# Kernel optimization log

Measured on AMD Instinct MI355X. Metric: run time of the kernel, lower is better.

Reference implementation:

```python
import jax, jax.numpy as jnp
import numpy as np

H = 8
DH = 64  # attention_head_size
HID = 512
NEG = -90000000000.0

def _lin(x, w, b):
    return x @ w + b

def _tfs(x):  # [N, HID] -> [H, N, DH]
    n = x.shape[0]
    return x.reshape(n, H, DH).transpose(1, 0, 2)

def _cross(q, ck, v, cv, mask, dw, db):
    # q: [H,N,DH], ck/cv: [H,M,DH], v: [H,N,DH], mask: [N,M]
    s = jnp.einsum('hnd,hmd->hnm', q, ck)
    s = s * mask[None, :, :] / jnp.sqrt(jnp.asarray(DH, s.dtype))
    s = jnp.where(s == 0.0, NEG, s)  # faithful zero->-inf hack
    p = jax.nn.softmax(s, axis=-1)
    ctx = v + jnp.einsum('hnm,hmd->hnd', p, cv)  # residual add of raw value
    n = ctx.shape[1]
    ctx = ctx.transpose(1, 0, 2).reshape(n, H * DH)
    return _lin(ctx, dw, db)

def setup_inputs() -> dict:
    key = jax.random.key(0)
    ks = jax.random.split(key, 24)
    N1, N2, D1 = 4096, 4096, 300
    d = {}
    d['h_head'] = jax.random.normal(ks[0], (N1, D1), jnp.float32)
    d['h_tail'] = jax.random.normal(ks[1], (N2, HID), jnp.float32)
    d['batch_head'] = jnp.sort(jax.random.randint(ks[2], (N1,), 0, 64))
    d['batch_tail'] = jnp.sort(jax.random.randint(ks[3], (N2,), 0, 64))
    def w(k, i, o):
        return jax.random.normal(k, (i, o), jnp.float32) / np.sqrt(i)
    d['map_w'] = w(ks[4], D1, HID); d['map_b'] = jnp.zeros((HID,), jnp.float32)
    names = ['q1', 'k1', 'v1', 'q2', 'k2', 'v2', 'd1', 'd2']
    for i, nm in enumerate(names):
        d[nm + '_w'] = w(ks[5 + i], HID, HID)
        d[nm + '_b'] = jnp.zeros((HID,), jnp.float32)
    return d

def reference(h_head, h_tail, batch_head, batch_tail,
              map_w, map_b,
              q1_w, q1_b, k1_w, k1_b, v1_w, v1_b,
              q2_w, q2_b, k2_w, k2_b, v2_w, v2_b,
              d1_w, d1_b, d2_w, d2_b):
    hh = _lin(h_head, map_w, map_b)  # n_dim1 != n_dim2 -> map
    q_h = _tfs(_lin(hh, q1_w, q1_b))
    k_h = _tfs(_lin(hh, k1_w, k1_b))
    v_h = _tfs(_lin(hh, v1_w, v1_b))
    q_t = _tfs(_lin(h_tail, q2_w, q2_b))
    k_t = _tfs(_lin(h_tail, k2_w, k2_b))
    v_t = _tfs(_lin(h_tail, v2_w, v2_b))
    mask = (batch_head[:, None] == batch_tail[None, :]).astype(jnp.float32)
    out_head = _cross(q_h, k_t, v_h, v_t, mask, d1_w, d1_b)
    out_tail = _cross(q_t, k_h, v_t, v_h, mask.T, d2_w, d2_b)
    return (out_head, out_tail)
```

## Files before the change

### kernel.cpp

```cpp
#include <hip/hip_runtime.h>
#include <hip/hip_bf16.h>
#include <math.h>


typedef __bf16 bf16x8 __attribute__((ext_vector_type(8)));
typedef float  f32x4  __attribute__((ext_vector_type(4)));

#define HID 512
#define NTOK 4096

#define AS1(p) ((const __attribute__((address_space(1))) void*)(p))
#define AS3(p) ((__attribute__((address_space(3))) void*)(p))

__device__ __forceinline__ void fold_tile(
    const float* __restrict__ Wf,
    const float* __restrict__ Mw,
    __bf16* __restrict__ F,
    int bx, int by, char* SMEM)
{
    __bf16* As = (__bf16*)SMEM;
    __bf16* Bs = (__bf16*)(SMEM + 8192);

    const int tid  = threadIdx.x;
    const int wave = tid >> 6;
    const int lane = tid & 63;
    const int quad = lane >> 4;
    const int l16  = lane & 15;
    const int wy   = wave >> 1;
    const int wx   = wave & 1;
    const int rowBase = by * 128;
    const int colBase = bx * 128;

    const int s_row = tid >> 2;
    const int s_gc  = (tid & 3) ^ ((s_row >> 1) & 3);
    const int a_jj  = tid >> 3;
    const int a_c16 = (tid & 7) * 16;
    const int a_cp  = a_jj >> 3;
    const int a_sub = a_jj & 7;

    f32x4 acc[4][4] = {};

    for (int i = 0; i < 16; ++i) {
        const int j0 = i * 32;
        __syncthreads();
        #pragma unroll
        for (int h = 0; h < 2; ++h) {
            int r = s_row + h * 64;
            int k = colBase + r;
            bf16x8 v;
            if (k < 300) {
                const float* p = &Mw[(size_t)k * 512 + j0 + s_gc * 8];
                float4 f0 = *(const float4*)p;
                float4 f1 = *(const float4*)(p + 4);
                v[0]=(__bf16)f0.x; v[1]=(__bf16)f0.y; v[2]=(__bf16)f0.z; v[3]=(__bf16)f0.w;
                v[4]=(__bf16)f1.x; v[5]=(__bf16)f1.y; v[6]=(__bf16)f1.z; v[7]=(__bf16)f1.w;
            } else {
                #pragma unroll
                for (int u = 0; u < 8; ++u) v[u] = (__bf16)0.f;
            }
            *(bf16x8*)&Bs[h * 2048 + tid * 8] = v;
        }
        {
            const float* p = &Wf[(size_t)(j0 + a_jj) * 512 + rowBase + a_c16];
            float4 f0 = *(const float4*)p;
            float4 f1 = *(const float4*)(p + 4);
            float4 f2 = *(const float4*)(p + 8);
            float4 f3 = *(const float4*)(p + 12);
            float vals[16] = {f0.x,f0.y,f0.z,f0.w, f1.x,f1.y,f1.z,f1.w,
                              f2.x,f2.y,f2.z,f2.w, f3.x,f3.y,f3.z,f3.w};
            #pragma unroll
            for (int u = 0; u < 16; ++u) {
                int r  = a_c16 + u;
                int cp = a_cp ^ ((r >> 1) & 3);
                As[r * 32 + cp * 8 + a_sub] = (__bf16)vals[u];
            }
        }
        __syncthreads();

        bf16x8 ar[4], br[4];
        #pragma unroll
        for (int ii = 0; ii < 4; ++ii) {
            const int ra = wy * 64 + ii * 16 + l16;
            ar[ii] = *(const bf16x8*)&As[ra * 32 + ((quad ^ ((ra >> 1) & 3)) << 3)];
        }
        #pragma unroll
        for (int jj = 0; jj < 4; ++jj) {
            const int rb = wx * 64 + jj * 16 + l16;
            br[jj] = *(const bf16x8*)&Bs[rb * 32 + ((quad ^ ((rb >> 1) & 3)) << 3)];
        }
        #pragma unroll
        for (int ii = 0; ii < 4; ++ii)
            #pragma unroll
            for (int jj = 0; jj < 4; ++jj)
                acc[ii][jj] = __builtin_amdgcn_mfma_f32_16x16x32_bf16(ar[ii], br[jj], acc[ii][jj], 0, 0, 0);
    }

    #pragma unroll
    for (int jj = 0; jj < 4; ++jj) {
        int col = colBase + wx * 64 + jj * 16 + l16;
        if (col < 320) {
            #pragma unroll
            for (int ii = 0; ii < 4; ++ii) {
                #pragma unroll
                for (int r = 0; r < 4; ++r) {
                    int row = rowBase + wy * 64 + ii * 16 + quad * 4 + r;
                    F[(size_t)row * 320 + col] = (__bf16)acc[ii][jj][r];
                }
            }
        }
    }
}

struct PrepArgs {
    const float* h_head; const float* h_tail;
    const int* bh; const int* bt;
    const float* map_w; const float* map_b;
    const float* qkvw[3]; const float* qkvb[3];
    const float* tsrc[5]; __bf16* tdst[5];
    __bf16* hh_bf; __bf16* ht_bf;
    __bf16* F[3];
    float* fb;
    int* ranges;
};

__global__ __launch_bounds__(256) void fused_prep(PrepArgs pa) {
    const int q = blockIdx.x, z = blockIdx.z, tid = threadIdx.x;
    __shared__ __align__(16) char SMEM[32768];

    if (z == 0) {
        if (q == 0 && tid < 128) {
            int b = tid & 63;
            const int* arr = (tid < 64) ? pa.bh : pa.bt;
            int base = (tid < 64) ? 0 : 128;
            int lo = 0, hi = NTOK;
            while (lo < hi) { int mid = (lo + hi) >> 1; if (arr[mid] < b) lo = mid + 1; else hi = mid; }
            int start = lo;
            lo = 0; hi = NTOK;
            while (lo < hi) { int mid = (lo + hi) >> 1; if (arr[mid] <= b) lo = mid + 1; else hi = mid; }
            pa.ranges[base + b] = start;
            pa.ranges[base + 64 + b] = lo;
        }
        for (int idx = tid; idx < 8 * 40; idx += 256) {
            int r   = q * 8 + idx / 40;
            int col = (idx % 40) * 8;
            bf16x8 v;
            if (col + 8 <= 300) {
                float4 f0 = *(const float4*)&pa.h_head[(size_t)r * 300 + col];
                float4 f1 = *(const float4*)&pa.h_head[(size_t)r * 300 + col + 4];
                v[0]=(__bf16)f0.x; v[1]=(__bf16)f0.y; v[2]=(__bf16)f0.z; v[3]=(__bf16)f0.w;
                v[4]=(__bf16)f1.x; v[5]=(__bf16)f1.y; v[6]=(__bf16)f1.z; v[7]=(__bf16)f1.w;
            } else if (col < 300) {
                float4 f0 = *(const float4*)&pa.h_head[(size_t)r * 300 + col];
                v[0]=(__bf16)f0.x; v[1]=(__bf16)f0.y; v[2]=(__bf16)f0.z; v[3]=(__bf16)f0.w;
                v[4]=(__bf16)0.f; v[5]=(__bf16)0.f; v[6]=(__bf16)0.f; v[7]=(__bf16)0.f;
            } else {
                #pragma unroll
                for (int j = 0; j < 8; ++j) v[j] = (__bf16)0.f;
            }
            *(bf16x8*)&pa.hh_bf[(size_t)r * 320 + col] = v;
        }
    } else if (z == 1) {
        for (int idx = tid; idx < 8 * 64; idx += 256) {
            int r   = q * 8 + (idx >> 6);
            int col = (idx & 63) * 8;
            float4 f0 = *(const float4*)&pa.h_tail[(size_t)r * 512 + col];
            float4 f1 = *(const float4*)&pa.h_tail[(size_t)r * 512 + col + 4];
            bf16x8 v;
            v[0]=(__bf16)f0.x; v[1]=(__bf16)f0.y; v[2]=(__bf16)f0.z; v[3]=(__bf16)f0.w;
            v[4]=(__bf16)f1.x; v[5]=(__bf16)f1.y; v[6]=(__bf16)f1.z; v[7]=(__bf16)f1.w;
            *(bf16x8*)&pa.ht_bf[(size_t)r * 512 + col] = v;
        }
    } else if (z == 2) {
        if (q >= 24) return;
        float* red = (float*)SMEM;
        const int w  = q >> 3;
        const int c8 = q & 7;
        const int n  = c8 * 64 + (tid & 63);
        const int jq = tid >> 6;
        const float* W = pa.qkvw[w];
        float s = 0.f;
        for (int j = jq * 128; j < jq * 128 + 128; ++j)
            s += pa.map_b[j] * W[(size_t)j * 512 + n];
        red[tid] = s;
        __syncthreads();
        if (tid < 64) {
            float r4 = red[tid] + red[64 + tid] + red[128 + tid] + red[192 + tid]
                     + pa.qkvb[w][c8 * 64 + tid];
            pa.fb[w * 512 + c8 * 64 + tid] = r4;
        }
    } else if (z == 3) {
        if (q >= 36) return;
        const int f = q / 12, t = q % 12;
        fold_tile(pa.qkvw[f], pa.map_w, pa.F[f], t % 3, t / 3, SMEM);
    } else {
        if (q >= 64) return;
        typedef __bf16 trow[72];
        trow* T = (trow*)SMEM;
        const int jz = z - 4;
        const float* src = pa.tsrc[jz];
        __bf16* dst = pa.tdst[jz];
        const int tk = (q >> 3) * 64;
        const int tn = (q & 7) * 64;
        const int r0 = tid >> 4;
        const int c0 = (tid & 15) * 4;
        #pragma unroll
        for (int i = 0; i < 4; ++i) {
            float4 v = *(const float4*)&src[(size_t)(tk + r0 + i * 16) * 512 + tn + c0];
            T[r0 + i * 16][c0 + 0] = (__bf16)v.x;
            T[r0 + i * 16][c0 + 1] = (__bf16)v.y;
            T[r0 + i * 16][c0 + 2] = (__bf16)v.z;
            T[r0 + i * 16][c0 + 3] = (__bf16)v.w;
        }
        __syncthreads();
        const int n  = tid >> 2;
        const int kk = (tid & 3) * 16;
        bf16x8 o0, o1;
        #pragma unroll
        for (int j = 0; j < 8; ++j) { o0[j] = T[kk + j][n]; o1[j] = T[kk + 8 + j][n]; }
        __bf16* dp = dst + (size_t)(tn + n) * 512 + tk + kk;
        *(bf16x8*)dp       = o0;
        *(bf16x8*)(dp + 8) = o1;
    }
}

struct GemmJobs {
    const __bf16* A[6];
    const __bf16* W[6];
    const float*  bias[6];
    void*         C[6];
    int           Kp[6];
};

template <typename TC>
__global__ __launch_bounds__(256) void gemm128(GemmJobs jobs) {
    __shared__ __align__(16) __bf16 As[2][4096];
    __shared__ __align__(16) __bf16 Bs[2][4096];

    const int z = blockIdx.z;
    const __bf16* A    = jobs.A[z];
    const __bf16* W    = jobs.W[z];
    const float*  bias = jobs.bias[z];
    TC*           C    = (TC*)jobs.C[z];
    const int     Kp   = jobs.Kp[z];

    const int tid  = threadIdx.x;
    const int wave = tid >> 6;
    const int lane = tid & 63;
    const int quad = lane >> 4;
    const int l16  = lane & 15;
    const int wy   = wave >> 1;
    const int wx   = wave & 1;
    const int rowBase = blockIdx.y * 128;
    const int colBase = blockIdx.x * 128;

    const int s_row = tid >> 2;
    const int s_kc  = ((tid & 3) ^ ((s_row >> 1) & 3)) * 8;

    const __bf16* gA = A + (size_t)(rowBase + s_row) * Kp + s_kc;
    const __bf16* gB = W + (size_t)(colBase + s_row) * Kp + s_kc;
    const int waveOff = wave * 512;

    f32x4 acc[4][4] = {};
    const int nk = Kp >> 5;

    __builtin_amdgcn_global_load_lds(AS1(gA),                   AS3(&As[0][waveOff]),        16, 0, 0);
    __builtin_amdgcn_global_load_lds(AS1(gA + (size_t)64 * Kp), AS3(&As[0][2048 + waveOff]), 16, 0, 0);
    __builtin_amdgcn_global_load_lds(AS1(gB),                   AS3(&Bs[0][waveOff]),        16, 0, 0);
    __builtin_amdgcn_global_load_lds(AS1(gB + (size_t)64 * Kp), AS3(&Bs[0][2048 + waveOff]), 16, 0, 0);

    for (int i = 0; i < nk; ++i) {
        const int cur = i & 1;
        __syncthreads();

        if (i + 1 < nk) {
            const int kt = (i + 1) * 32;
            const int nx = cur ^ 1;
            __builtin_amdgcn_global_load_lds(AS1(gA + kt),                   AS3(&As[nx][waveOff]),        16, 0, 0);
            __builtin_amdgcn_global_load_lds(AS1(gA + kt + (size_t)64 * Kp), AS3(&As[nx][2048 + waveOff]), 16, 0, 0);
            __builtin_amdgcn_global_load_lds(AS1(gB + kt),                   AS3(&Bs[nx][waveOff]),        16, 0, 0);
            __builtin_amdgcn_global_load_lds(AS1(gB + kt + (size_t)64 * Kp), AS3(&Bs[nx][2048 + waveOff]), 16, 0, 0);
        }

        bf16x8 ar[4], br[4];
        #pragma unroll
        for (int ii = 0; ii < 4; ++ii) {
            const int ra = wy * 64 + ii * 16 + l16;
            ar[ii] = *(const bf16x8*)&As[cur][ra * 32 + ((quad ^ ((ra >> 1) & 3)) << 3)];
        }
        #pragma unroll
        for (int jj = 0; jj < 4; ++jj) {
            const int rb = wx * 64 + jj * 16 + l16;
            br[jj] = *(const bf16x8*)&Bs[cur][rb * 32 + ((quad ^ ((rb >> 1) & 3)) << 3)];
        }
        #pragma unroll
        for (int ii = 0; ii < 4; ++ii)
            #pragma unroll
            for (int jj = 0; jj < 4; ++jj)
                acc[ii][jj] = __builtin_amdgcn_mfma_f32_16x16x32_bf16(ar[ii], br[jj], acc[ii][jj], 0, 0, 0);
    }

    #pragma unroll
    for (int jj = 0; jj < 4; ++jj) {
        int col = colBase + wx * 64 + jj * 16 + l16;
        float bv = bias[col];
        #pragma unroll
        for (int ii = 0; ii < 4; ++ii) {
            #pragma unroll
            for (int r = 0; r < 4; ++r) {
                int row = rowBase + wy * 64 + ii * 16 + quad * 4 + r;
                C[(size_t)row * HID + col] = (TC)(acc[ii][jj][r] + bv);
            }
        }
    }
}

__global__ __launch_bounds__(256) void attn_mfma(
    const __bf16* __restrict__ Q0, const __bf16* __restrict__ K0,
    const __bf16* __restrict__ Vr0, const __bf16* __restrict__ Vc0,
    const __bf16* __restrict__ Q1, const __bf16* __restrict__ K1,
    const __bf16* __restrict__ Vr1, const __bf16* __restrict__ Vc1,
    const int* __restrict__ ranges,
    __bf16* __restrict__ O0, __bf16* __restrict__ O1,
    int Nq, int Nk)
{
    __shared__ __align__(16) __bf16 Qs[64][72];
    __shared__ __align__(16) __bf16 Ks[64][72];
    __shared__ __align__(16) __bf16 Vt[64][72];
    __shared__ __align__(16) __bf16 Ps[64][72];

    const int z = blockIdx.z;
    const __bf16* Q    = z ? Q1 : Q0;
    const __bf16* Kg   = z ? K1 : K0;
    const __bf16* Vres = z ? Vr1 : Vr0;
    const __bf16* Vctx = z ? Vc1 : Vc0;
    __bf16* Out        = z ? O1 : O0;
    const int* qstart  = z ? ranges + 128 : ranges;
    const int* qend    = z ? ranges + 192 : ranges + 64;
    const int* kstart  = z ? ranges       : ranges + 128;
    const int* kend    = z ? ranges + 64  : ranges + 192;

    const int h = blockIdx.x, b = blockIdx.y;
    const int qs = qstart[b], qe = qend[b];
    const int ts = kstart[b], te = kend[b];
    const int nq = qe - qs, nk = te - ts;
    if (nq <= 0) return;

    const int tid  = threadIdx.x;
    const int wave = tid >> 6;
    const int lane = tid & 63;
    const int quad = lane >> 4;
    const int l16  = lane & 15;
    const int srow = tid >> 2;
    const int scol = (tid & 3) * 16;

    if (nk <= 0) {
        float* meanv = (float*)Qs;
        if (tid < 64) {
            float s = 0.f;
            for (int m = 0; m < Nk; ++m)
                s += (float)Vctx[(size_t)m * HID + h * 64 + tid];
            meanv[tid] = s / (float)Nk;
        }
        __syncthreads();
        int d = tid & 63;
        for (int r = qs + (tid >> 6); r < qe; r += 4) {
            size_t off = (size_t)r * HID + h * 64 + d;
            Out[off] = (__bf16)((float)Vres[off] + meanv[d]);
        }
        return;
    }

    for (int qc = 0; qc < nq; qc += 64) {
        __syncthreads();
        {
            int qg = min(qs + qc + srow, Nq - 1);
            const __bf16* src = Q + (size_t)qg * HID + h * 64 + scol;
            *(bf16x8*)&Qs[srow][scol]     = *(const bf16x8*)src;
            *(bf16x8*)&Qs[srow][scol + 8] = *(const bf16x8*)(src + 8);
        }
        __syncthreads();
        bf16x8 aq0 = *(const bf16x8*)&Qs[wave * 16 + l16][quad * 8];
        bf16x8 aq1 = *(const bf16x8*)&Qs[wave * 16 + l16][32 + quad * 8];

        f32x4 O[4] = {};
        float Mx[4], L[4];
        #pragma unroll
        for (int r = 0; r < 4; ++r) { Mx[r] = -__builtin_inff(); L[r] = 0.f; }

        for (int kc = 0; kc < nk; kc += 64) {
            __syncthreads();
            {
                int kg = min(ts + kc + srow, Nk - 1);
                const __bf16* ksrc = Kg + (size_t)kg * HID + h * 64 + scol;
                *(bf16x8*)&Ks[srow][scol]     = *(const bf16x8*)ksrc;
                *(bf16x8*)&Ks[srow][scol + 8] = *(const bf16x8*)(ksrc + 8);
                const __bf16* vsrc = Vctx + (size_t)kg * HID + h * 64 + scol;
                bf16x8 v0 = *(const bf16x8*)vsrc;
                bf16x8 v1 = *(const bf16x8*)(vsrc + 8);
                #pragma unroll
                for (int j = 0; j < 8; ++j) {
                    Vt[scol + j][srow]     = v0[j];
                    Vt[scol + 8 + j][srow] = v1[j];
                }
            }
            __syncthreads();

            f32x4 S[4] = {};
            #pragma unroll
            for (int c = 0; c < 4; ++c) {
                bf16x8 bk0 = *(const bf16x8*)&Ks[c * 16 + l16][quad * 8];
                bf16x8 bk1 = *(const bf16x8*)&Ks[c * 16 + l16][32 + quad * 8];
                S[c] = __builtin_amdgcn_mfma_f32_16x16x32_bf16(aq0, bk0, S[c], 0, 0, 0);
                S[c] = __builtin_amdgcn_mfma_f32_16x16x32_bf16(aq1, bk1, S[c], 0, 0, 0);
            }

            #pragma unroll
            for (int c = 0; c < 4; ++c) {
                bool valid = (ts + kc + c * 16 + l16) < te;
                #pragma unroll
                for (int r = 0; r < 4; ++r)
                    S[c][r] = valid ? S[c][r] * 0.125f : -__builtin_inff();
            }

            float cm[4], ps[4], alpha[4];
            #pragma unroll
            for (int r = 0; r < 4; ++r) {
                float v = fmaxf(fmaxf(S[0][r], S[1][r]), fmaxf(S[2][r], S[3][r]));
                v = fmaxf(v, __shfl_xor(v, 1, 64));
                v = fmaxf(v, __shfl_xor(v, 2, 64));
                v = fmaxf(v, __shfl_xor(v, 4, 64));
                v = fmaxf(v, __shfl_xor(v, 8, 64));
                cm[r] = v;
            }
            #pragma unroll
            for (int r = 0; r < 4; ++r) {
                float nM = fmaxf(Mx[r], cm[r]);
                alpha[r] = __expf(Mx[r] - nM);
                Mx[r] = nM;
                ps[r] = 0.f;
            }
            #pragma unroll
            for (int c = 0; c < 4; ++c)
                #pragma unroll
                for (int r = 0; r < 4; ++r) {
                    float p = __expf(S[c][r] - Mx[r]);
                    S[c][r] = p;
                    ps[r] += p;
                }
            #pragma unroll
            for (int r = 0; r < 4; ++r) {
                float v = ps[r];
                v += __shfl_xor(v, 1, 64);
                v += __shfl_xor(v, 2, 64);
                v += __shfl_xor(v, 4, 64);
                v += __shfl_xor(v, 8, 64);
                L[r] = L[r] * alpha[r] + v;
            }
            #pragma unroll
            for (int c = 0; c < 4; ++c)
                #pragma unroll
                for (int r = 0; r < 4; ++r)
                    O[c][r] *= alpha[r];

            #pragma unroll
            for (int c = 0; c < 4; ++c)
                #pragma unroll
                for (int r = 0; r < 4; ++r)
                    Ps[wave * 16 + quad * 4 + r][c * 16 + l16] = (__bf16)S[c][r];
            __syncthreads();

            bf16x8 ap0 = *(const bf16x8*)&Ps[wave * 16 + l16][quad * 8];
            bf16x8 ap1 = *(const bf16x8*)&Ps[wave * 16 + l16][32 + quad * 8];
            #pragma unroll
            for (int c = 0; c < 4; ++c) {
                bf16x8 bv0 = *(const bf16x8*)&Vt[c * 16 + l16][quad * 8];
                bf16x8 bv1 = *(const bf16x8*)&Vt[c * 16 + l16][32 + quad * 8];
                O[c] = __builtin_amdgcn_mfma_f32_16x16x32_bf16(ap0, bv0, O[c], 0, 0, 0);
                O[c] = __builtin_amdgcn_mfma_f32_16x16x32_bf16(ap1, bv1, O[c], 0, 0, 0);
            }
        }

        #pragma unroll
        for (int c = 0; c < 4; ++c) {
            int d = h * 64 + c * 16 + l16;
            #pragma unroll
            for (int r = 0; r < 4; ++r) {
                int qrow = qs + qc + wave * 16 + quad * 4 + r;
                if (qrow < qe) {
                    size_t off = (size_t)qrow * HID + d;
                    Out[off] = (__bf16)((float)Vres[off] + O[c][r] / L[r]);
                }
            }
        }
    }
}

extern "C" void kernel_launch(void* const* d_in, const int* in_sizes, int n_in,
                              void* d_out, int out_size, void* d_ws, size_t ws_size,
                              hipStream_t stream) {
    (void)in_sizes; (void)n_in; (void)out_size; (void)ws_size;

    const float* h_head = (const float*)d_in[0];
    const float* h_tail = (const float*)d_in[1];
    const int* batch_head = (const int*)d_in[2];
    const int* batch_tail = (const int*)d_in[3];
    const float* map_w = (const float*)d_in[4];
    const float* map_b = (const float*)d_in[5];
    const float* q1_w = (const float*)d_in[6];
    const float* q1_b = (const float*)d_in[7];
    const float* k1_w = (const float*)d_in[8];
    const float* k1_b = (const float*)d_in[9];
    const float* v1_w = (const float*)d_in[10];
    const float* v1_b = (const float*)d_in[11];
    const float* q2_w = (const float*)d_in[12];
    const float* q2_b = (const float*)d_in[13];
    const float* k2_w = (const float*)d_in[14];
    const float* k2_b = (const float*)d_in[15];
    const float* v2_w = (const float*)d_in[16];
    const float* v2_b = (const float*)d_in[17];
    const float* d1_w = (const float*)d_in[18];
    const float* d1_b = (const float*)d_in[19];
    const float* d2_w = (const float*)d_in[20];
    const float* d2_b = (const float*)d_in[21];

    float* out = (float*)d_out;

    const size_t SZ = (size_t)NTOK * HID;
    char* ws = (char*)d_ws;
    int* ranges   = (int*)ws;
    __bf16* hh_bf = (__bf16*)(ws + 1024);
    __bf16* ht_bf = hh_bf + (size_t)NTOK * 320;
    __bf16* q2T  = ht_bf + SZ;
    __bf16* k2T  = q2T + 512 * 512;
    __bf16* v2T  = k2T + 512 * 512;
    __bf16* d1T  = v2T + 512 * 512;
    __bf16* d2T  = d1T + 512 * 512;
    __bf16* FqT  = d2T + 512 * 512;
    __bf16* FkT  = FqT + 512 * 320;
    __bf16* FvT  = FkT + 512 * 320;
    __bf16* qh   = FvT + 512 * 320;
    __bf16* kh   = qh  + SZ;
    __bf16* vh   = kh  + SZ;
    __bf16* qt   = vh  + SZ;
    __bf16* kt   = qt  + SZ;
    __bf16* vt   = kt  + SZ;
    __bf16* ctxh = vt  + SZ;
    __bf16* ctxt = ctxh + SZ;
    float*  fb   = (float*)(ctxt + SZ);

    PrepArgs pa;
    pa.h_head = h_head; pa.h_tail = h_tail;
    pa.bh = batch_head; pa.bt = batch_tail;
    pa.map_w = map_w; pa.map_b = map_b;
    pa.qkvw[0] = q1_w; pa.qkvw[1] = k1_w; pa.qkvw[2] = v1_w;
    pa.qkvb[0] = q1_b; pa.qkvb[1] = k1_b; pa.qkvb[2] = v1_b;
    const float* wsrc[5] = {q2_w, k2_w, v2_w, d1_w, d2_w};
    __bf16* wdst[5] = {q2T, k2T, v2T, d1T, d2T};
    for (int i = 0; i < 5; ++i) { pa.tsrc[i] = wsrc[i]; pa.tdst[i] = wdst[i]; }
    pa.hh_bf = hh_bf; pa.ht_bf = ht_bf;
    pa.F[0] = FqT; pa.F[1] = FkT; pa.F[2] = FvT;
    pa.fb = fb; pa.ranges = ranges;
    fused_prep<<<dim3(512, 1, 9), dim3(256), 0, stream>>>(pa);

    {
        GemmJobs j;
        j.A[0] = hh_bf; j.W[0] = FqT; j.bias[0] = fb;        j.C[0] = qh; j.Kp[0] = 320;
        j.A[1] = hh_bf; j.W[1] = FkT; j.bias[1] = fb + 512;  j.C[1] = kh; j.Kp[1] = 320;
        j.A[2] = hh_bf; j.W[2] = FvT; j.bias[2] = fb + 1024; j.C[2] = vh; j.Kp[2] = 320;
        j.A[3] = ht_bf; j.W[3] = q2T; j.bias[3] = q2_b;      j.C[3] = qt; j.Kp[3] = 512;
        j.A[4] = ht_bf; j.W[4] = k2T; j.bias[4] = k2_b;      j.C[4] = kt; j.Kp[4] = 512;
        j.A[5] = ht_bf; j.W[5] = v2T; j.bias[5] = v2_b;      j.C[5] = vt; j.Kp[5] = 512;
        gemm128<__bf16><<<dim3(4, 32, 6), dim3(256), 0, stream>>>(j);
    }

    attn_mfma<<<dim3(8, 64, 2), dim3(256), 0, stream>>>(
        qh, kt, vh, vt,
        qt, kh, vt, vh,
        ranges, ctxh, ctxt, NTOK, NTOK);

    {
        GemmJobs j;
        j.A[0] = ctxh; j.W[0] = d1T; j.bias[0] = d1_b; j.C[0] = out;      j.Kp[0] = 512;
        j.A[1] = ctxt; j.W[1] = d2T; j.bias[1] = d2_b; j.C[1] = out + SZ; j.Kp[1] = 512;
        j.A[2] = ctxt; j.W[2] = d2T; j.bias[2] = d2_b; j.C[2] = out + SZ; j.Kp[2] = 512;
        j.A[3] = ctxt; j.W[3] = d2T; j.bias[3] = d2_b; j.C[3] = out + SZ; j.Kp[3] = 512;
        j.A[4] = ctxt; j.W[4] = d2T; j.bias[4] = d2_b; j.C[4] = out + SZ; j.Kp[4] = 512;
        j.A[5] = ctxt; j.W[5] = d2T; j.bias[5] = d2_b; j.C[5] = out + SZ; j.Kp[5] = 512;
        gemm128<float><<<dim3(4, 32, 2), dim3(256), 0, stream>>>(j);
    }
}
```

Baseline: 198.3 us.

## Fold map bias into padded K column and prefetch fold-tile loads

```diff
diff --git a/kernel.cpp b/kernel.cpp
--- a/kernel.cpp
+++ b/kernel.cpp
@@ -4,6 +4,7 @@
 
 
 typedef __bf16 bf16x8 __attribute__((ext_vector_type(8)));
+typedef __bf16 bf16x4 __attribute__((ext_vector_type(4)));
 typedef float  f32x4  __attribute__((ext_vector_type(4)));
 
 #define HID 512
@@ -15,6 +16,7 @@
 __device__ __forceinline__ void fold_tile(
     const float* __restrict__ Wf,
     const float* __restrict__ Mw,
+    const float* __restrict__ Mb,
     __bf16* __restrict__ F,
     int bx, int by, char* SMEM)
 {
@@ -33,48 +35,64 @@
 
     const int s_row = tid >> 2;
     const int s_gc  = (tid & 3) ^ ((s_row >> 1) & 3);
-    const int a_jj  = tid >> 3;
-    const int a_c16 = (tid & 7) * 16;
-    const int a_cp  = a_jj >> 3;
-    const int a_sub = a_jj & 7;
+    const int a_j4 = (tid & 7) * 4;
+    const int a_n4 = (tid >> 3) * 4;
+
+    float aR[16];
+    float4 b0lo, b0hi, b1lo, b1hi;
+
+    auto loadA = [&](int j0) {
+        #pragma unroll
+        for (int u = 0; u < 4; ++u)
+            *(float4*)&aR[u * 4] =
+                *(const float4*)&Wf[(size_t)(j0 + a_j4 + u) * 512 + rowBase + a_n4];
+    };
+    auto loadRow = [&](int k, int jc, float4& lo, float4& hi) {
+        if (k < 300) {
+            lo = *(const float4*)&Mw[(size_t)k * 512 + jc];
+            hi = *(const float4*)&Mw[(size_t)k * 512 + jc + 4];
+        } else if (k == 300) {
+            lo = *(const float4*)&Mb[jc];
+            hi = *(const float4*)&Mb[jc + 4];
+        } else {
+            lo = float4{0.f, 0.f, 0.f, 0.f};
+            hi = float4{0.f, 0.f, 0.f, 0.f};
+        }
+    };
+    auto loadB = [&](int j0) {
+        const int jc = j0 + s_gc * 8;
+        loadRow(colBase + s_row,      jc, b0lo, b0hi);
+        loadRow(colBase + 64 + s_row, jc, b1lo, b1hi);
+    };
 
     f32x4 acc[4][4] = {};
 
+    loadA(0);
+    loadB(0);
+
     for (int i = 0; i < 16; ++i) {
-        const int j0 = i * 32;
-        __syncthreads();
-        #pragma unroll
-        for (int h = 0; h < 2; ++h) {
-            int r = s_row + h * 64;
-            int k = colBase + r;
-            bf16x8 v;
-            if (k < 300) {
-                const float* p = &Mw[(size_t)k * 512 + j0 + s_gc * 8];
-                float4 f0 = *(const float4*)p;
-                float4 f1 = *(const float4*)(p + 4);
-                v[0]=(__bf16)f0.x; v[1]=(__bf16)f0.y; v[2]=(__bf16)f0.z; v[3]=(__bf16)f0.w;
-                v[4]=(__bf16)f1.x; v[5]=(__bf16)f1.y; v[6]=(__bf16)f1.z; v[7]=(__bf16)f1.w;
-            } else {
-                #pragma unroll
-                for (int u = 0; u < 8; ++u) v[u] = (__bf16)0.f;
-            }
-            *(bf16x8*)&Bs[h * 2048 + tid * 8] = v;
+        __syncthreads();
+        #pragma unroll
+        for (int v = 0; v < 4; ++v) {
+            const int r = a_n4 + v;
+            const int p = (a_j4 >> 3) ^ ((r >> 1) & 3);
+            bf16x4 w;
+            w[0] = (__bf16)aR[0 * 4 + v];
+            w[1] = (__bf16)aR[1 * 4 + v];
+            w[2] = (__bf16)aR[2 * 4 + v];
+            w[3] = (__bf16)aR[3 * 4 + v];
+            *(bf16x4*)&As[r * 32 + p * 8 + (a_j4 & 7)] = w;
         }
         {
-            const float* p = &Wf[(size_t)(j0 + a_jj) * 512 + rowBase + a_c16];
-            float4 f0 = *(const float4*)p;
-            float4 f1 = *(const float4*)(p + 4);
-            float4 f2 = *(const float4*)(p + 8);
-            float4 f3 = *(const float4*)(p + 12);
-            float vals[16] = {f0.x,f0.y,f0.z,f0.w, f1.x,f1.y,f1.z,f1.w,
-                              f2.x,f2.y,f2.z,f2.w, f3.x,f3.y,f3.z,f3.w};
-            #pragma unroll
-            for (int u = 0; u < 16; ++u) {
-                int r  = a_c16 + u;
-                int cp = a_cp ^ ((r >> 1) & 3);
-                As[r * 32 + cp * 8 + a_sub] = (__bf16)vals[u];
-            }
-        }
+            bf16x8 v0, v1;
+            v0[0]=(__bf16)b0lo.x; v0[1]=(__bf16)b0lo.y; v0[2]=(__bf16)b0lo.z; v0[3]=(__bf16)b0lo.w;
+            v0[4]=(__bf16)b0hi.x; v0[5]=(__bf16)b0hi.y; v0[6]=(__bf16)b0hi.z; v0[7]=(__bf16)b0hi.w;
+            v1[0]=(__bf16)b1lo.x; v1[1]=(__bf16)b1lo.y; v1[2]=(__bf16)b1lo.z; v1[3]=(__bf16)b1lo.w;
+            v1[4]=(__bf16)b1hi.x; v1[5]=(__bf16)b1hi.y; v1[6]=(__bf16)b1hi.z; v1[7]=(__bf16)b1hi.w;
+            *(bf16x8*)&Bs[tid * 8]        = v0;
+            *(bf16x8*)&Bs[2048 + tid * 8] = v1;
+        }
+        if (i + 1 < 16) { loadA((i + 1) * 32); loadB((i + 1) * 32); }
         __syncthreads();
 
         bf16x8 ar[4], br[4];
@@ -115,17 +133,16 @@
     const float* h_head; const float* h_tail;
     const int* bh; const int* bt;
     const float* map_w; const float* map_b;
-    const float* qkvw[3]; const float* qkvb[3];
+    const float* qkvw[3];
     const float* tsrc[5]; __bf16* tdst[5];
     __bf16* hh_bf; __bf16* ht_bf;
     __bf16* F[3];
-    float* fb;
     int* ranges;
 };
 
 __global__ __launch_bounds__(256) void fused_prep(PrepArgs pa) {
     const int q = blockIdx.x, z = blockIdx.z, tid = threadIdx.x;
-    __shared__ __align__(16) char SMEM[32768];
+    __shared__ __align__(16) char SMEM[16384];
 
     if (z == 0) {
         if (q == 0 && tid < 128) {
@@ -152,7 +169,8 @@
             } else if (col < 300) {
                 float4 f0 = *(const float4*)&pa.h_head[(size_t)r * 300 + col];
                 v[0]=(__bf16)f0.x; v[1]=(__bf16)f0.y; v[2]=(__bf16)f0.z; v[3]=(__bf16)f0.w;
-                v[4]=(__bf16)0.f; v[5]=(__bf16)0.f; v[6]=(__bf16)0.f; v[7]=(__bf16)0.f;
+                v[4]=(__bf16)1.0f;
+                v[5]=(__bf16)0.f; v[6]=(__bf16)0.f; v[7]=(__bf16)0.f;
             } else {
                 #pragma unroll
                 for (int j = 0; j < 8; ++j) v[j] = (__bf16)0.f;
@@ -171,32 +189,14 @@
             *(bf16x8*)&pa.ht_bf[(size_t)r * 512 + col] = v;
         }
     } else if (z == 2) {
-        if (q >= 24) return;
-        float* red = (float*)SMEM;
-        const int w  = q >> 3;
-        const int c8 = q & 7;
-        const int n  = c8 * 64 + (tid & 63);
-        const int jq = tid >> 6;
-        const float* W = pa.qkvw[w];
-        float s = 0.f;
-        for (int j = jq * 128; j < jq * 128 + 128; ++j)
-            s += pa.map_b[j] * W[(size_t)j * 512 + n];
-        red[tid] = s;
-        __syncthreads();
-        if (tid < 64) {
-            float r4 = red[tid] + red[64 + tid] + red[128 + tid] + red[192 + tid]
-                     + pa.qkvb[w][c8 * 64 + tid];
-            pa.fb[w * 512 + c8 * 64 + tid] = r4;
-        }
-    } else if (z == 3) {
         if (q >= 36) return;
         const int f = q / 12, t = q % 12;
-        fold_tile(pa.qkvw[f], pa.map_w, pa.F[f], t % 3, t / 3, SMEM);
+        fold_tile(pa.qkvw[f], pa.map_w, pa.map_b, pa.F[f], t % 3, t / 3, SMEM);
     } else {
         if (q >= 64) return;
         typedef __bf16 trow[72];
         trow* T = (trow*)SMEM;
-        const int jz = z - 4;
+        const int jz = z - 3;
         const float* src = pa.tsrc[jz];
         __bf16* dst = pa.tdst[jz];
         const int tk = (q >> 3) * 64;
@@ -546,30 +546,28 @@
     __bf16* vt   = kt  + SZ;
     __bf16* ctxh = vt  + SZ;
     __bf16* ctxt = ctxh + SZ;
-    float*  fb   = (float*)(ctxt + SZ);
 
     PrepArgs pa;
     pa.h_head = h_head; pa.h_tail = h_tail;
     pa.bh = batch_head; pa.bt = batch_tail;
     pa.map_w = map_w; pa.map_b = map_b;
     pa.qkvw[0] = q1_w; pa.qkvw[1] = k1_w; pa.qkvw[2] = v1_w;
-    pa.qkvb[0] = q1_b; pa.qkvb[1] = k1_b; pa.qkvb[2] = v1_b;
     const float* wsrc[5] = {q2_w, k2_w, v2_w, d1_w, d2_w};
     __bf16* wdst[5] = {q2T, k2T, v2T, d1T, d2T};
     for (int i = 0; i < 5; ++i) { pa.tsrc[i] = wsrc[i]; pa.tdst[i] = wdst[i]; }
     pa.hh_bf = hh_bf; pa.ht_bf = ht_bf;
     pa.F[0] = FqT; pa.F[1] = FkT; pa.F[2] = FvT;
-    pa.fb = fb; pa.ranges = ranges;
-    fused_prep<<<dim3(512, 1, 9), dim3(256), 0, stream>>>(pa);
+    pa.ranges = ranges;
+    fused_prep<<<dim3(512, 1, 8), dim3(256), 0, stream>>>(pa);
 
     {
         GemmJobs j;
-        j.A[0] = hh_bf; j.W[0] = FqT; j.bias[0] = fb;        j.C[0] = qh; j.Kp[0] = 320;
-        j.A[1] = hh_bf; j.W[1] = FkT; j.bias[1] = fb + 512;  j.C[1] = kh; j.Kp[1] = 320;
-        j.A[2] = hh_bf; j.W[2] = FvT; j.bias[2] = fb + 1024; j.C[2] = vh; j.Kp[2] = 320;
-        j.A[3] = ht_bf; j.W[3] = q2T; j.bias[3] = q2_b;      j.C[3] = qt; j.Kp[3] = 512;
-        j.A[4] = ht_bf; j.W[4] = k2T; j.bias[4] = k2_b;      j.C[4] = kt; j.Kp[4] = 512;
-        j.A[5] = ht_bf; j.W[5] = v2T; j.bias[5] = v2_b;      j.C[5] = vt; j.Kp[5] = 512;
+        j.A[0] = hh_bf; j.W[0] = FqT; j.bias[0] = q1_b; j.C[0] = qh; j.Kp[0] = 320;
+        j.A[1] = hh_bf; j.W[1] = FkT; j.bias[1] = k1_b; j.C[1] = kh; j.Kp[1] = 320;
+        j.A[2] = hh_bf; j.W[2] = FvT; j.bias[2] = v1_b; j.C[2] = vh; j.Kp[2] = 320;
+        j.A[3] = ht_bf; j.W[3] = q2T; j.bias[3] = q2_b; j.C[3] = qt; j.Kp[3] = 512;
+        j.A[4] = ht_bf; j.W[4] = k2T; j.bias[4] = k2_b; j.C[4] = kt; j.Kp[4] = 512;
+        j.A[5] = ht_bf; j.W[5] = v2T; j.bias[5] = v2_b; j.C[5] = vt; j.Kp[5] = 512;
         gemm128<__bf16><<<dim3(4, 32, 6), dim3(256), 0, stream>>>(j);
     }
 
```

Result: faster. 184.0 us (-7.2%).
